# Optimization experiments

Measured on AMD Instinct MI355X. Metric: run time of the kernel, lower is better.

Reference implementation:

```python
import jax, jax.numpy as jnp
import numpy as np
import math

DIM = 128
D_STATE = 16
D_CONV = 4
EXPAND = 2
LFS = 16            # last_feat_size -> H = W = 16, L = 256
IN_IMG = 512
IN_PC = 256
COMB = IN_IMG + IN_PC + 2          # 770
POOL_SCALES = [1, 5, 9, 13]        # arithmetic(1, 16, 4)
NPOOL = len(POOL_SCALES)
D_MODEL = DIM * NPOOL + COMB       # 1282
D_INNER = EXPAND * D_MODEL         # 2564
DT_RANK = math.ceil(D_MODEL / 16)  # 81
B = 64
H = W = LFS


def _ap_mat(insz, outsz):
    # PyTorch AdaptiveAvgPool2d bin weights as a (outsz, insz) matrix
    M = np.zeros((outsz, insz), np.float32)
    for i in range(outsz):
        s = (i * insz) // outsz
        e = -((-(i + 1) * insz) // outsz)  # ceil((i+1)*insz/outsz)
        M[i, s:e] = 1.0 / (e - s)
    return M


def _bl_mat(outsz, insz):
    # bilinear interpolation (align_corners=False) as (outsz, insz) matrix
    M = np.zeros((outsz, insz), np.float32)
    if insz == 1:
        M[:, 0] = 1.0
        return M
    for i in range(outsz):
        src = (i + 0.5) * insz / outsz - 0.5
        src = min(max(src, 0.0), insz - 1.0)
        i0 = int(np.floor(src))
        i1 = min(i0 + 1, insz - 1)
        f = src - i0
        M[i, i0] += 1.0 - f
        M[i, i1] += f
    return M


def setup_inputs():
    key = jax.random.key(0)
    ks = jax.random.split(key, 16)
    def n(k, sh, s=1.0):
        return jax.random.normal(k, sh, jnp.float32) * s
    return {
        'x': n(ks[0], (B, IN_IMG, H, W)),
        'pc_emb': n(ks[1], (B, IN_PC)),
        'conv_w': n(ks[2], (NPOOL, DIM, COMB), 0.05),          # 1x1 convs
        'bn_gamma': jnp.ones((NPOOL, DIM), jnp.float32),
        'bn_beta': jnp.zeros((NPOOL, DIM), jnp.float32),
        'bn_mean': n(ks[3], (NPOOL, DIM), 0.1),
        'bn_var': jax.random.uniform(ks[4], (NPOOL, DIM), jnp.float32, 0.5, 1.5),
        'in_proj_w': n(ks[5], (2 * D_INNER, D_MODEL), D_MODEL ** -0.5),
        'conv1d_w': n(ks[6], (D_INNER, 1, D_CONV), 0.3),       # depthwise causal conv
        'conv1d_b': n(ks[7], (D_INNER,), 0.1),
        'x_proj_w': n(ks[8], (DT_RANK + 2 * D_STATE, D_INNER), D_INNER ** -0.5),
        'dt_proj_w': n(ks[9], (D_INNER, DT_RANK), DT_RANK ** -0.5),
        'dt_proj_b': n(ks[10], (D_INNER,), 0.5) - 3.0,
        'A_log': jnp.log(jax.random.uniform(ks[11], (D_INNER, D_STATE), jnp.float32, 1.0, 16.0)),
        'D': jnp.ones((D_INNER,), jnp.float32),
        'out_proj_w': n(ks[12], (D_MODEL, D_INNER), D_INNER ** -0.5),
    }


def _ppm(x, pc_emb, conv_w, bn_gamma, bn_beta, bn_mean, bn_var):
    Bn = x.shape[0]
    xx = np.linspace(-0.3, 0.3, LFS, dtype=np.float32)
    g = np.stack(np.meshgrid(xx, xx)).reshape(2, LFS, LFS)
    grid = jnp.broadcast_to(jnp.asarray(g)[None], (Bn, 2, H, W))
    pc = jnp.broadcast_to(pc_emb[:, :, None, None], (Bn, IN_PC, H, W))
    comb = jnp.concatenate([x, grid, pc], axis=1)  # (B, COMB, H, W)

    def cbr(i, t):  # 1x1 conv -> BN(eval) -> ReLU6
        y = jnp.einsum('bchw,dc->bdhw', t, conv_w[i])
        inv = jax.lax.rsqrt(bn_var[i] + 1e-5) * bn_gamma[i]
        y = y * inv[None, :, None, None] + (bn_beta[i] - bn_mean[i] * inv)[None, :, None, None]
        return jnp.clip(y, 0.0, 6.0)

    outs = [comb]
    # pool layer 0: ConvBNReLU then AdaptiveAvgPool2d(1); bilinear from 1x1 = broadcast
    y0 = cbr(0, comb).mean(axis=(2, 3), keepdims=True)
    outs.append(jnp.broadcast_to(y0, (Bn, DIM, H, W)))
    for i, s in enumerate(POOL_SCALES[1:], start=1):
        Mp = jnp.asarray(_ap_mat(H, s))
        pooled = jnp.einsum('oh,bchw,pw->bcop', Mp, comb, Mp)  # adaptive avg pool
        y = cbr(i, pooled)
        Mu = jnp.asarray(_bl_mat(H, s))
        outs.append(jnp.einsum('oh,bchw,pw->bcop', Mu, y, Mu))  # bilinear upsample
    return jnp.concatenate(outs, axis=1)  # (B, D_MODEL, H, W)


def _mamba(seq, in_proj_w, conv1d_w, conv1d_b, x_proj_w, dt_proj_w, dt_proj_b, A_log, D, out_proj_w):
    # seq: (B, L, d_model)
    xz = seq @ in_proj_w.T                       # (B, L, 2*d_inner)
    u, z = jnp.split(xz, 2, axis=-1)
    uc = jnp.transpose(u, (0, 2, 1))             # (B, d_inner, L)
    uc = jax.lax.conv_general_dilated(uc, conv1d_w, (1,), [(D_CONV - 1, 0)],
                                      feature_group_count=D_INNER) + conv1d_b[None, :, None]
    u = jax.nn.silu(jnp.transpose(uc, (0, 2, 1)))  # (B, L, d_inner)
    dbl = u @ x_proj_w.T
    dt, Bm, Cm = jnp.split(dbl, [DT_RANK, DT_RANK + D_STATE], axis=-1)
    dt = jax.nn.softplus(dt @ dt_proj_w.T + dt_proj_b)  # (B, L, d_inner)
    A = -jnp.exp(A_log)                                 # (d_inner, d_state)

    def step(h, inp):
        dt_t, B_t, C_t, u_t = inp                # (B,d_inner) (B,N) (B,N) (B,d_inner)
        dA = jnp.exp(dt_t[..., None] * A)        # (B, d_inner, N)
        h = dA * h + (dt_t * u_t)[..., None] * B_t[:, None, :]
        y = jnp.einsum('bdn,bn->bd', h, C_t)
        return h, y

    h0 = jnp.zeros((seq.shape[0], D_INNER, D_STATE), seq.dtype)
    xs = (jnp.moveaxis(dt, 1, 0), jnp.moveaxis(Bm, 1, 0),
          jnp.moveaxis(Cm, 1, 0), jnp.moveaxis(u, 1, 0))
    _, ys = jax.lax.scan(step, h0, xs)
    y = jnp.moveaxis(ys, 0, 1) + u * D
    y = y * jax.nn.silu(z)
    return y @ out_proj_w.T                      # (B, L, d_model)


def reference(x, pc_emb, conv_w, bn_gamma, bn_beta, bn_mean, bn_var,
              in_proj_w, conv1d_w, conv1d_b, x_proj_w, dt_proj_w, dt_proj_b,
              A_log, D, out_proj_w):
    Bn = x.shape[0]
    feat = _ppm(x, pc_emb, conv_w, bn_gamma, bn_beta, bn_mean, bn_var)
    chs = feat.shape[1]
    seq = jnp.transpose(feat.reshape(Bn, chs, H * W), (0, 2, 1))  # b (h w) c
    y = _mamba(seq, in_proj_w, conv1d_w, conv1d_b, x_proj_w,
               dt_proj_w, dt_proj_b, A_log, D, out_proj_w)
    return jnp.transpose(y, (0, 2, 1)).reshape(Bn, chs, H, W)
```

## Files before the change

kernel.cpp:

```cpp
#include <hip/hip_runtime.h>
#include <hip/hip_bf16.h>
#include <math.h>

#define H_ 16
#define W_ 16
#define L_ 256
#define BATCH 64
#define CIMG 512
#define CPC 256
#define COMB_ 770
#define DIMC 128
#define DMODEL 1282
#define DINNER 2564
#define DXZ 5128
#define DTRANK 81
#define NSTATE 16
#define NPOS 275

#define KP_IN 928
#define KBASE 384
#define KP_OUT 2592
#define KP_DT 96
#define NPAD_IN 5248
#define NPAD_OUT 1408
#define NPAD_X 128
#define NPAD_DT 2688
#define XSPLIT 9

typedef __attribute__((ext_vector_type(8))) short short8;
typedef __attribute__((ext_vector_type(4))) float f32x4;

__device__ __forceinline__ float comb_val(const float* __restrict__ x,
                                          const float* __restrict__ pc,
                                          int bg, int c, int h, int w) {
  if (c < CIMG)    return x[(((size_t)bg * CIMG + c) << 8) + (h << 4) + w];
  if (c == CIMG)   return -0.3f + 0.04f * (float)w;
  if (c == CIMG+1) return -0.3f + 0.04f * (float)h;
  return pc[bg * CPC + (c - (CIMG + 2))];
}

__device__ __forceinline__ void split_bf16(float v, unsigned short& h, unsigned short& l) {
  __hip_bfloat16 hb = __float2bfloat16(v);
  h = __builtin_bit_cast(unsigned short, hb);
  float r = v - __bfloat162float(hb);
  __hip_bfloat16 lb = __float2bfloat16(r);
  l = __builtin_bit_cast(unsigned short, lb);
}

__device__ __forceinline__ float bf16_val(unsigned short u) {
  return __bfloat162float(__builtin_bit_cast(__hip_bfloat16, u));
}

__device__ __forceinline__ void idx_to_scale(int idx, int& s, int& o, int& p, int& base) {
  if (idx < 25)       { s = 5;  base = 0; }
  else if (idx < 106) { s = 9;  base = 25; }
  else                { s = 13; base = 106; }
  int r = idx - base;
  o = r / s; p = r - o * s;
}

__global__ __launch_bounds__(256) void wsplit_kernel(
    const float* __restrict__ W, int N, int K,
    unsigned short* __restrict__ Wh, unsigned short* __restrict__ Wl, int Kp) {
  int k = blockIdx.x * 256 + threadIdx.x;
  if (k >= Kp) return;
  int n = blockIdx.y;
  float v = (n < N && k < K) ? W[(size_t)n * K + k] : 0.f;
  unsigned short h, l;
  split_bf16(v, h, l);
  Wh[(size_t)n * Kp + k] = h;
  Wl[(size_t)n * Kp + k] = l;
}

__global__ __launch_bounds__(256) void wsplit_main_kernel(
    const float* __restrict__ W,
    unsigned short* __restrict__ Wh, unsigned short* __restrict__ Wl) {
  int k = blockIdx.x * 256 + threadIdx.x;
  if (k >= KP_IN) return;
  int n = blockIdx.y;
  float v = 0.f;
  if (n < DXZ && k < 898) {
    int src = (k < 514) ? k : k + 384;
    v = W[(size_t)n * DMODEL + src];
  }
  unsigned short h, l;
  split_bf16(v, h, l);
  Wh[(size_t)n * KP_IN + k] = h;
  Wl[(size_t)n * KP_IN + k] = l;
}

__global__ __launch_bounds__(256) void wsplit_base_kernel(
    const float* __restrict__ W,
    unsigned short* __restrict__ Wh, unsigned short* __restrict__ Wl) {
  int k = blockIdx.x * 256 + threadIdx.x;
  if (k >= KBASE) return;
  int n = blockIdx.y;
  float v = (n < DXZ) ? W[(size_t)n * DMODEL + 514 + k] : 0.f;
  unsigned short h, l;
  split_bf16(v, h, l);
  Wh[(size_t)n * KBASE + k] = h;
  Wl[(size_t)n * KBASE + k] = l;
}

__global__ __launch_bounds__(128) void wt_kernel(
    const float* __restrict__ cw, float* __restrict__ Wt) {
  int c = blockIdx.x, i = blockIdx.y, d = threadIdx.x;
  Wt[((size_t)i * COMB_ + c) * DIMC + d] = cw[((size_t)i * DIMC + d) * COMB_ + c];
}

__global__ __launch_bounds__(256) void pool_kernel(
    const float* __restrict__ x, const float* __restrict__ pc,
    float* __restrict__ P, int b0) {
  int t = blockIdx.x * 256 + threadIdx.x;
  if (t >= COMB_ * NPOS) return;
  int bl = blockIdx.y;
  int bg = b0 + bl;
  int c = t / NPOS;
  int idx = t - c * NPOS;
  int s, o, p, base; idx_to_scale(idx, s, o, p, base);
  int hs = (o * 16) / s, he = ((o + 1) * 16 + s - 1) / s;
  int ws2 = (p * 16) / s, we = ((p + 1) * 16 + s - 1) / s;
  float sum = 0.f;
  for (int h = hs; h < he; h++)
    for (int w = ws2; w < we; w++)
      sum += comb_val(x, pc, bg, c, h, w);
  P[((size_t)bl * COMB_ + c) * NPOS + idx] = sum / (float)((he - hs) * (we - ws2));
}

__global__ __launch_bounds__(256) void cbr_pool_a_kernel(
    const float* __restrict__ P, const float* __restrict__ Wt,
    float* __restrict__ Ypar) {
  int tno = blockIdx.x, cg = blockIdx.y, bl = blockIdx.z;
  int i, idx0, cnt;
  if (tno == 0)      { i = 0; idx0 = 0;                cnt = 25; }
  else if (tno < 4)  { i = 1; idx0 = 25 + (tno-1)*32;  cnt = min(32, 106 - idx0); }
  else               { i = 2; idx0 = 106 + (tno-4)*32; cnt = min(32, 275 - idx0); }
  int cbeg = (cg * COMB_) >> 2, cend_ = ((cg + 1) * COMB_) >> 2;
  __shared__ float Ps[64][32];
  __shared__ float Ws[64][128];
  int t = threadIdx.x;
  int dg = t & 31, ig = t >> 5;
  int d0 = dg << 2, ii0 = ig << 2;
  float acc[4][4] = {};
  for (int c0 = cbeg; c0 < cend_; c0 += 64) {
    int cend = min(64, cend_ - c0);
    for (int e = t; e < 64 * 32; e += 256) {
      int cc = e >> 5, ii = e & 31;
      float v = 0.f;
      if (cc < cend && ii < cnt)
        v = P[((size_t)bl * COMB_ + c0 + cc) * NPOS + idx0 + ii];
      Ps[cc][ii] = v;
    }
    for (int e = t; e < 64 * 128; e += 256) {
      int cc = e >> 7, dd = e & 127;
      Ws[cc][dd] = (cc < cend) ? Wt[((size_t)(i + 1) * COMB_ + c0 + cc) * DIMC + dd] : 0.f;
    }
    __syncthreads();
    for (int cc = 0; cc < 64; cc++) {
      f32x4 wv = *(const f32x4*)&Ws[cc][d0];
      f32x4 pv = *(const f32x4*)&Ps[cc][ii0];
      #pragma unroll
      for (int di = 0; di < 4; di++)
        #pragma unroll
        for (int ki = 0; ki < 4; ki++)
          acc[di][ki] += wv[di] * pv[ki];
    }
    __syncthreads();
  }
  size_t cgs = (size_t)cg * BATCH * NPOS * DIMC;
  #pragma unroll
  for (int di = 0; di < 4; di++) {
    #pragma unroll
    for (int ki = 0; ki < 4; ki++) {
      int io = ii0 + ki;
      if (io < cnt)
        Ypar[cgs + ((size_t)bl * NPOS + idx0 + io) * DIMC + d0 + di] = acc[di][ki];
    }
  }
}

__global__ __launch_bounds__(128) void cbr_comb_kernel(
    const float* __restrict__ Ypar,
    const float* __restrict__ gamma, const float* __restrict__ beta,
    const float* __restrict__ mean, const float* __restrict__ var,
    float* __restrict__ Y) {
  int idx = blockIdx.x, bl = blockIdx.y, d = threadIdx.x;
  int i = (idx < 25) ? 1 : (idx < 106 ? 2 : 3);
  size_t cgs = (size_t)BATCH * NPOS * DIMC;
  size_t o = ((size_t)bl * NPOS + idx) * DIMC + d;
  float v = Ypar[o] + Ypar[o + cgs] + Ypar[o + 2 * cgs] + Ypar[o + 3 * cgs];
  int bi = i * DIMC + d;
  float inv = rsqrtf(var[bi] + 1e-5f) * gamma[bi];
  v = v * inv + (beta[bi] - mean[bi] * inv);
  Y[o] = fminf(fmaxf(v, 0.f), 6.f);
}

__global__ __launch_bounds__(256) void cbr0a_kernel(
    const float* __restrict__ x, const float* __restrict__ pc,
    const float* __restrict__ Wt, float* __restrict__ y0c) {
  int tile = blockIdx.x, bl = blockIdx.y;
  int lt = tile & 3, cg = tile >> 2;
  int cbeg = (cg * COMB_) >> 2, cend_ = ((cg + 1) * COMB_) >> 2;
  __shared__ float Cs[64][64];
  __shared__ float Ws[64][128];
  int t = threadIdx.x;
  int dg = t & 31, lg = t >> 5;
  int d0 = dg << 2, l0 = lg << 3;
  float acc[4][8] = {};
  for (int c0 = cbeg; c0 < cend_; c0 += 64) {
    int cn = min(64, cend_ - c0);
    for (int e = t; e < 64 * 64; e += 256) {
      int cc = e >> 6, ll = e & 63;
      float v = 0.f;
      if (cc < cn) {
        int l = lt * 64 + ll;
        v = comb_val(x, pc, bl, c0 + cc, l >> 4, l & 15);
      }
      Cs[cc][ll] = v;
    }
    for (int e = t; e < 64 * 128; e += 256) {
      int cc = e >> 7, dd = e & 127;
      Ws[cc][dd] = (cc < cn) ? Wt[(size_t)(c0 + cc) * DIMC + dd] : 0.f;
    }
    __syncthreads();
    for (int cc = 0; cc < 64; cc++) {
      f32x4 wv = *(const f32x4*)&Ws[cc][d0];
      f32x4 pa = *(const f32x4*)&Cs[cc][l0];
      f32x4 pb = *(const f32x4*)&Cs[cc][l0 + 4];
      #pragma unroll
      for (int di = 0; di < 4; di++) {
        #pragma unroll
        for (int li = 0; li < 4; li++) {
          acc[di][li]     += wv[di] * pa[li];
          acc[di][li + 4] += wv[di] * pb[li];
        }
      }
    }
    __syncthreads();
  }
  #pragma unroll
  for (int di = 0; di < 4; di++)
    #pragma unroll
    for (int li = 0; li < 8; li++)
      y0c[(((size_t)bl * 4 + cg) * 256 + lt * 64 + l0 + li) * DIMC + d0 + di] =
          acc[di][li];
}

__global__ __launch_bounds__(256) void cbr0b_kernel(
    const float* __restrict__ y0c,
    const float* __restrict__ gamma, const float* __restrict__ beta,
    const float* __restrict__ mean, const float* __restrict__ var,
    float* __restrict__ y0s) {
  int bl = blockIdx.x;
  int t = threadIdx.x;
  int d = t & 127, lh = t >> 7;
  float inv = rsqrtf(var[d] + 1e-5f) * gamma[d];
  float bs = beta[d] - mean[d] * inv;
  float s = 0.f;
  size_t cgs = (size_t)256 * DIMC;
  for (int l = lh * 128; l < lh * 128 + 128; l++) {
    size_t base = (((size_t)bl * 4) * 256 + l) * DIMC + d;
    float v = y0c[base] + y0c[base + cgs] + y0c[base + 2 * cgs] + y0c[base + 3 * cgs];
    v = v * inv + bs;
    s += fminf(fmaxf(v, 0.f), 6.f);
  }
  __shared__ float red[256];
  red[t] = s;
  __syncthreads();
  if (t < 128) y0s[bl * DIMC + t] = red[t] + red[t + 128];
}

__global__ __launch_bounds__(256) void pcy0_kernel(
    const float* __restrict__ pc, const float* __restrict__ y0s,
    unsigned short* __restrict__ Abh, unsigned short* __restrict__ Abl) {
  int k = blockIdx.x * 256 + threadIdx.x;
  if (k >= KBASE) return;
  int row = blockIdx.y;
  float v = 0.f;
  if (row < BATCH) {
    if (k < CPC) v = pc[row * CPC + k];
    else v = y0s[(size_t)row * DIMC + (k - CPC)] * (1.f / 256.f);
  }
  unsigned short h, l;
  split_bf16(v, h, l);
  Abh[(size_t)row * KBASE + k] = h;
  Abl[(size_t)row * KBASE + k] = l;
}

__global__ __launch_bounds__(256) void seq_x_kernel(
    const float* __restrict__ x,
    unsigned short* __restrict__ seqh, unsigned short* __restrict__ seql, int b0) {
  int ct = blockIdx.x, ltile = blockIdx.y, bl = blockIdx.z;
  int bg = b0 + bl;
  __shared__ float Ct[64][65];
  int t = threadIdx.x;
  int c0 = ct << 6, l0 = ltile << 6;
  for (int e = t; e < 64 * 64; e += 256) {
    int cc = e >> 6, ll = e & 63;
    Ct[ll][cc] = x[(((size_t)bg * CIMG + c0 + cc) << 8) + l0 + ll];
  }
  __syncthreads();
  int r = t >> 2, cq = (t & 3) << 4;
  size_t rb = ((size_t)bl * L_ + l0 + r) * KP_IN + c0 + cq;
  short8 h0, h1, lo0, lo1;
  #pragma unroll
  for (int k = 0; k < 8; k++) {
    unsigned short hh, ll;
    split_bf16(Ct[r][cq + k], hh, ll);
    h0[k] = (short)hh; lo0[k] = (short)ll;
  }
  #pragma unroll
  for (int k = 0; k < 8; k++) {
    unsigned short hh, ll;
    split_bf16(Ct[r][cq + 8 + k], hh, ll);
    h1[k] = (short)hh; lo1[k] = (short)ll;
  }
  *(short8*)&seqh[rb]     = h0;
  *(short8*)&seqh[rb + 8] = h1;
  *(short8*)&seql[rb]     = lo0;
  *(short8*)&seql[rb + 8] = lo1;
}

__global__ __launch_bounds__(256) void seq_rest_kernel(
    const float* __restrict__ x, const float* __restrict__ pc,
    const float* __restrict__ Y,
    unsigned short* __restrict__ seqh, unsigned short* __restrict__ seql, int b0) {
  int l = blockIdx.x, bl = blockIdx.y, bg = b0 + bl;
  int h = l >> 4, w = l & 15;
  size_t rb = ((size_t)bl * L_ + l) * KP_IN;
  for (int c = 512 + threadIdx.x; c < KP_IN; c += 256) {
    float v;
    if (c < CIMG + 2) {
      v = comb_val(x, pc, bg, c, h, w);
    } else if (c < 898) {
      int cc = c - 514;
      int si = cc >> 7;
      int d = cc & 127;
      int s    = (si == 0) ? 5 : ((si == 1) ? 9 : 13);
      int base = (si == 0) ? 0 : ((si == 1) ? 25 : 106);
      float srch = (h + 0.5f) * (float)s * (1.f / 16.f) - 0.5f;
      srch = fminf(fmaxf(srch, 0.f), (float)(s - 1));
      int o0 = (int)floorf(srch);
      float fh = srch - (float)o0;
      int o1 = min(o0 + 1, s - 1);
      float srcw = (w + 0.5f) * (float)s * (1.f / 16.f) - 0.5f;
      srcw = fminf(fmaxf(srcw, 0.f), (float)(s - 1));
      int p0 = (int)floorf(srcw);
      float fw = srcw - (float)p0;
      int p1 = min(p0 + 1, s - 1);
      const float* Yb = &Y[((size_t)bg * NPOS + base) * DIMC + d];
      float v00 = Yb[(size_t)(o0 * s + p0) * DIMC];
      float v01 = Yb[(size_t)(o0 * s + p1) * DIMC];
      float v10 = Yb[(size_t)(o1 * s + p0) * DIMC];
      float v11 = Yb[(size_t)(o1 * s + p1) * DIMC];
      v = (1.f - fh) * ((1.f - fw) * v00 + fw * v01)
        +        fh  * ((1.f - fw) * v10 + fw * v11);
    } else {
      v = 0.f;
    }
    unsigned short hh, ll;
    split_bf16(v, hh, ll);
    seqh[rb + c] = hh;
    seql[rb + c] = ll;
  }
}

__global__ __launch_bounds__(256) void mfma_gemm_kernel(
    const unsigned short* __restrict__ Ah, const unsigned short* __restrict__ Al, int Kp,
    const unsigned short* __restrict__ Bh, const unsigned short* __restrict__ Bl,
    float* __restrict__ C, int ldc, int M, int N, int mode,
    const float* __restrict__ bias,
    float* __restrict__ outT, int b0, size_t czstr) {
  __shared__ __align__(16) unsigned short Sbuf[2][4][128 * 32];
  int tid = threadIdx.x;
  int lane = tid & 63;
  int wave = tid >> 6;

  int kn = Kp / (int)gridDim.z;
  int kbeg = (int)blockIdx.z * kn;
  int nt = kn >> 5;
  C += (size_t)blockIdx.z * czstr;

  int gx = gridDim.x, gy = gridDim.y;
  int lin = blockIdx.y * gx + blockIdx.x;
  int total = gx * gy;
  int mt, nt_;
  if ((total & 7) == 0) {
    int vid = (lin & 7) * (total >> 3) + (lin >> 3);
    mt = vid % gy; nt_ = vid / gy;
  } else {
    mt = blockIdx.y; nt_ = blockIdx.x;
  }
  int m0 = mt << 7, n0 = nt_ << 7;
  int wm = (wave & 1) << 6, wn = (wave >> 1) << 6;
  f32x4 acc[4][4] = {};
  int mrow = lane & 15;
  int kx = (((lane >> 4) ^ ((lane >> 2) & 3)) << 3);

  auto STAGE = [&](int ph, int k0) {
    #pragma unroll
    for (int j = 0; j < 2; j++) {
      int c = (j << 8) + tid;
      int r = c >> 2;
      int kc = (((c & 3) ^ ((r >> 2) & 3)) << 3);
      size_t ga = (size_t)(m0 + r) * Kp + k0 + kc;
      size_t gb = (size_t)(n0 + r) * Kp + k0 + kc;
      __builtin_amdgcn_global_load_lds(
          (const __attribute__((address_space(1))) unsigned int*)(Ah + ga),
          (__attribute__((address_space(3))) unsigned int*)(&Sbuf[ph][0][c << 3]), 16, 0, 0);
      __builtin_amdgcn_global_load_lds(
          (const __attribute__((address_space(1))) unsigned int*)(Al + ga),
          (__attribute__((address_space(3))) unsigned int*)(&Sbuf[ph][1][c << 3]), 16, 0, 0);
      __builtin_amdgcn_global_load_lds(
          (const __attribute__((address_space(1))) unsigned int*)(Bh + gb),
          (__attribute__((address_space(3))) unsigned int*)(&Sbuf[ph][2][c << 3]), 16, 0, 0);
      __builtin_amdgcn_global_load_lds(
          (const __attribute__((address_space(1))) unsigned int*)(Bl + gb),
          (__attribute__((address_space(3))) unsigned int*)(&Sbuf[ph][3][c << 3]), 16, 0, 0);
    }
  };

  STAGE(0, kbeg);
  __syncthreads();
  int cur = 0;
  for (int t = 0; t < nt; t++) {
    if (t + 1 < nt) STAGE(cur ^ 1, kbeg + ((t + 1) << 5));
    short8 ah[4], al[4], bh[4], blo[4];
    #pragma unroll
    for (int i = 0; i < 4; i++) {
      int ro = (wm + (i << 4) + mrow) * 32 + kx;
      ah[i] = *(const short8*)&Sbuf[cur][0][ro];
      al[i] = *(const short8*)&Sbuf[cur][1][ro];
    }
    #pragma unroll
    for (int j = 0; j < 4; j++) {
      int ro = (wn + (j << 4) + mrow) * 32 + kx;
      bh[j]  = *(const short8*)&Sbuf[cur][2][ro];
      blo[j] = *(const short8*)&Sbuf[cur][3][ro];
    }
    #pragma unroll
    for (int i = 0; i < 4; i++)
      #pragma unroll
      for (int j = 0; j < 4; j++) {
        acc[i][j] = __builtin_amdgcn_mfma_f32_16x16x32_bf16(ah[i], bh[j],  acc[i][j], 0, 0, 0);
        acc[i][j] = __builtin_amdgcn_mfma_f32_16x16x32_bf16(ah[i], blo[j], acc[i][j], 0, 0, 0);
        acc[i][j] = __builtin_amdgcn_mfma_f32_16x16x32_bf16(al[i], bh[j],  acc[i][j], 0, 0, 0);
      }
    __syncthreads();
    cur ^= 1;
  }

  int n_l = lane & 15, m_l = (lane >> 4) << 2;
  #pragma unroll
  for (int i = 0; i < 4; i++) {
    int gm0 = m0 + wm + (i << 4) + m_l;
    #pragma unroll
    for (int j = 0; j < 4; j++) {
      int gn = n0 + wn + (j << 4) + n_l;
      if (gn >= N) continue;
      if (mode == 2) {
        int bb = b0 + (gm0 >> 8), l0 = gm0 & 255;
        *(f32x4*)&outT[(((size_t)bb * DMODEL + gn) << 8) + l0] = acc[i][j];
      } else if (mode == 1) {
        float bv = bias[gn];
        #pragma unroll
        for (int r = 0; r < 4; r++) {
          float vv = acc[i][j][r] + bv;
          vv = (vv > 20.f) ? vv : log1pf(expf(vv));
          C[(size_t)(gm0 + r) * ldc + gn] = vv;
        }
      } else if (mode == 3) {
        float bv = bias[(size_t)(b0 + (gm0 >> 8)) * DXZ + gn];
        if (gn < DINNER) {
          #pragma unroll
          for (int r = 0; r < 4; r++)
            C[(size_t)(gm0 + r) * DINNER + gn] = acc[i][j][r] + bv;
        } else {
          int g2 = gn - DINNER;
          #pragma unroll
          for (int r = 0; r < 4; r++)
            outT[(size_t)(gm0 + r) * DINNER + g2] = acc[i][j][r] + bv;
        }
      } else {
        #pragma unroll
        for (int r = 0; r < 4; r++)
          C[(size_t)(gm0 + r) * ldc + gn] = acc[i][j][r];
      }
    }
  }
}

__global__ __launch_bounds__(256) void conv1d_kernel(
    const float* __restrict__ U, const float* __restrict__ cw,
    const float* __restrict__ cb,
    unsigned short* __restrict__ vh, unsigned short* __restrict__ vl) {
  int d = blockIdx.x * 256 + threadIdx.x;
  if (d >= KP_OUT) return;
  int m0 = blockIdx.y << 2;
  if (d >= DINNER) {
    #pragma unroll
    for (int q = 0; q < 4; q++) {
      size_t o = (size_t)(m0 + q) * KP_OUT + d;
      vh[o] = 0; vl[o] = 0;
    }
    return;
  }
  int bbase = m0 & ~255;
  float xr[7];
  #pragma unroll
  for (int k = 0; k < 7; k++) {
    int r = m0 - 3 + k;
    xr[k] = (r >= bbase) ? U[(size_t)r * DINNER + d] : 0.f;
  }
  float w0 = cw[d * 4], w1 = cw[d * 4 + 1], w2 = cw[d * 4 + 2], w3 = cw[d * 4 + 3];
  float b = cb[d];
  #pragma unroll
  for (int q = 0; q < 4; q++) {
    float acc = b + w0 * xr[q] + w1 * xr[q + 1] + w2 * xr[q + 2] + w3 * xr[q + 3];
    float s = acc / (1.f + __expf(-acc));
    unsigned short hh, llv;
    split_bf16(s, hh, llv);
    size_t o = (size_t)(m0 + q) * KP_OUT + d;
    vh[o] = hh; vl[o] = llv;
  }
}

__global__ __launch_bounds__(256) void split_bc_kernel(
    const float* __restrict__ dbl, size_t zstr,
    unsigned short* __restrict__ dth, unsigned short* __restrict__ dtl,
    float* __restrict__ bcs, int Mtot) {
  int t = blockIdx.x * 256 + threadIdx.x;
  int m = t >> 7, k = t & 127;
  if (m >= Mtot) return;
  const float* p = dbl + (size_t)m * 128;
  if (k < KP_DT) {
    float v = 0.f;
    if (k < DTRANK) {
      #pragma unroll
      for (int q = 0; q < XSPLIT; q++) v += p[(size_t)q * zstr + k];
    }
    unsigned short h, l;
    split_bf16(v, h, l);
    dth[(size_t)m * KP_DT + k] = h;
    dtl[(size_t)m * KP_DT + k] = l;
  } else {
    int n = k - KP_DT;
    float v = 0.f;
    #pragma unroll
    for (int q = 0; q < XSPLIT; q++) v += p[(size_t)q * zstr + DTRANK + n];
    bcs[(size_t)m * 32 + n] = v;
  }
}

__global__ __launch_bounds__(256) void scan_kernel(
    const float* __restrict__ dtv,
    const unsigned short* __restrict__ vh, const unsigned short* __restrict__ vl,
    const float* __restrict__ Z,
    const float* __restrict__ bcs, const float* __restrict__ A_log,
    const float* __restrict__ Dv,
    unsigned short* __restrict__ yh, unsigned short* __restrict__ yl) {
  int dl = threadIdx.x & 63;
  int s  = threadIdx.x >> 6;
  int d  = (blockIdx.x << 6) + dl;
  int bl = blockIdx.y;
  bool valid = d < DINNER;
  bool wout  = d < KP_OUT;
  int de = valid ? d : (DINNER - 1);
  __shared__ float Sh[3][64][NSTATE];
  __shared__ float Sp[3][64][NSTATE];
  float A[NSTATE], h[NSTATE];
  #pragma unroll
  for (int n = 0; n < NSTATE; n++) {
    A[n] = -__expf(A_log[de * NSTATE + n]);
    h[n] = 0.f;
  }
  float Dd = Dv[de];
  size_t mb = (size_t)bl * L_ + (s << 6);
  if (s < 3) {
    float sdt = 0.f;
    for (int i = 0; i < 64; i++) {
      size_t m = mb + i;
      float dt = dtv[m * DINNER + de];
      float uu = bf16_val(vh[m * KP_OUT + de]) + bf16_val(vl[m * KP_OUT + de]);
      const f32x4* bp = (const f32x4*)&bcs[m * 32];
      f32x4 b4a = bp[0], b4b = bp[1], b4c = bp[2], b4d = bp[3];
      float du = dt * uu;
      sdt += dt;
      #pragma unroll
      for (int n = 0; n < NSTATE; n++) {
        float bv = (n < 4) ? b4a[n & 3] : (n < 8) ? b4b[n & 3]
                 : (n < 12) ? b4c[n & 3] : b4d[n & 3];
        h[n] = __expf(dt * A[n]) * h[n] + du * bv;
      }
    }
    #pragma unroll
    for (int n = 0; n < NSTATE; n++) {
      Sh[s][dl][n] = h[n];
      Sp[s][dl][n] = __expf(A[n] * sdt);
    }
  }
  __syncthreads();
  #pragma unroll
  for (int n = 0; n < NSTATE; n++) h[n] = 0.f;
  for (int t = 0; t < s; t++)
    #pragma unroll
    for (int n = 0; n < NSTATE; n++)
      h[n] = Sp[t][dl][n] * h[n] + Sh[t][dl][n];
  for (int i = 0; i < 64; i++) {
    size_t m = mb + i;
    float dt = dtv[m * DINNER + de];
    float uu = bf16_val(vh[m * KP_OUT + de]) + bf16_val(vl[m * KP_OUT + de]);
    float zz = Z[m * DINNER + de];
    const f32x4* bp = (const f32x4*)&bcs[m * 32];
    f32x4 b4a = bp[0], b4b = bp[1], b4c = bp[2], b4d = bp[3];
    f32x4 c4a = bp[4], c4b = bp[5], c4c = bp[6], c4d = bp[7];
    float du = dt * uu;
    float y = 0.f;
    #pragma unroll
    for (int n = 0; n < NSTATE; n++) {
      float bv = (n < 4) ? b4a[n & 3] : (n < 8) ? b4b[n & 3]
               : (n < 12) ? b4c[n & 3] : b4d[n & 3];
      float cv = (n < 4) ? c4a[n & 3] : (n < 8) ? c4b[n & 3]
               : (n < 12) ? c4c[n & 3] : c4d[n & 3];
      h[n] = __expf(dt * A[n]) * h[n] + du * bv;
      y += h[n] * cv;
    }
    float val = (y + uu * Dd) * (zz / (1.f + __expf(-zz)));
    if (!valid) val = 0.f;
    if (wout) {
      unsigned short hh, ll;
      split_bf16(val, hh, ll);
      yh[m * KP_OUT + d] = hh;
      yl[m * KP_OUT + d] = ll;
    }
  }
}

extern "C" void kernel_launch(void* const* d_in, const int* in_sizes, int n_in,
                              void* d_out, int out_size, void* d_ws, size_t ws_size,
                              hipStream_t stream) {
  const float* x         = (const float*)d_in[0];
  const float* pc        = (const float*)d_in[1];
  const float* conv_w    = (const float*)d_in[2];
  const float* bn_gamma  = (const float*)d_in[3];
  const float* bn_beta   = (const float*)d_in[4];
  const float* bn_mean   = (const float*)d_in[5];
  const float* bn_var    = (const float*)d_in[6];
  const float* in_proj_w = (const float*)d_in[7];
  const float* conv1d_w  = (const float*)d_in[8];
  const float* conv1d_b  = (const float*)d_in[9];
  const float* x_proj_w  = (const float*)d_in[10];
  const float* dt_proj_w = (const float*)d_in[11];
  const float* dt_proj_b = (const float*)d_in[12];
  const float* A_log     = (const float*)d_in[13];
  const float* Dvec      = (const float*)d_in[14];
  const float* out_proj_w= (const float*)d_in[15];
  float* out = (float*)d_out;

  auto al = [](size_t vv) { return (vv + 255) & ~(size_t)255; };

  size_t w_in_sz  = al((size_t)NPAD_IN * KP_IN * 2);
  size_t w_b_sz   = al((size_t)NPAD_IN * KBASE * 2);
  size_t w_out_sz = al((size_t)NPAD_OUT * KP_OUT * 2);
  size_t w_x_sz   = al((size_t)NPAD_X * KP_OUT * 2);
  size_t w_d_sz   = al((size_t)NPAD_DT * KP_DT * 2);
  size_t wt_sz    = al((size_t)4 * COMB_ * DIMC * 4);
  size_t y0s_sz   = al((size_t)BATCH * DIMC * 4);
  size_t ab_sz    = al((size_t)128 * KBASE * 2);
  size_t cb_sz    = al((size_t)128 * DXZ * 4);
  size_t yf_sz    = al((size_t)BATCH * NPOS * DIMC * 4);
  size_t p_sz     = al((size_t)BATCH * COMB_ * NPOS * 4);
  size_t y0c_sz   = al((size_t)BATCH * 4 * 256 * DIMC * 4);
  size_t ypar_sz  = al((size_t)4 * BATCH * NPOS * DIMC * 4);

  char* base = (char*)d_ws;
  size_t off = 0;
  auto take = [&](size_t sz) { void* r = base + off; off += sz; return r; };
  unsigned short* Wih = (unsigned short*)take(w_in_sz);
  unsigned short* Wil = (unsigned short*)take(w_in_sz);
  unsigned short* Wbh = (unsigned short*)take(w_b_sz);
  unsigned short* Wbl = (unsigned short*)take(w_b_sz);
  unsigned short* Woh = (unsigned short*)take(w_out_sz);
  unsigned short* Wol = (unsigned short*)take(w_out_sz);
  unsigned short* Wxh = (unsigned short*)take(w_x_sz);
  unsigned short* Wxl = (unsigned short*)take(w_x_sz);
  unsigned short* Wdh = (unsigned short*)take(w_d_sz);
  unsigned short* Wdl = (unsigned short*)take(w_d_sz);
  float* Wt    = (float*)take(wt_sz);
  float* y0s   = (float*)take(y0s_sz);
  unsigned short* Abh = (unsigned short*)take(ab_sz);
  unsigned short* Abl = (unsigned short*)take(ab_sz);
  float* Cbase = (float*)take(cb_sz);
  float* Yf    = (float*)take(yf_sz);
  char* arena  = base + off;

  size_t pro_need = p_sz + y0c_sz + ypar_sz;
  auto chunk = [&](int bc) -> size_t {
    size_t Mcb = (size_t)bc * L_;
    size_t hyb = al(Mcb * KP_OUT * 2);
    size_t s = 2 * hyb
             + 2 * al(Mcb * DINNER * 4)
             + 2 * al(Mcb * KP_OUT * 2)
             + al((size_t)XSPLIT * Mcb * 128 * 4)
             + al(Mcb * 32 * 4)
             + 2 * al(Mcb * KP_DT * 2);
    return s < pro_need ? pro_need : s;
  };
  int Bc = 64;
  while (Bc > 1 && off + chunk(Bc) > ws_size) Bc >>= 1;

  size_t Mc = (size_t)Bc * L_;
  size_t hy = al(Mc * KP_OUT * 2);
  size_t zstr = Mc * 128;
  size_t aoff = 0;
  auto takeA = [&](size_t sz) { void* r = arena + aoff; aoff += sz; return r; };
  float* P    = (float*)arena;
  float* y0c  = (float*)(arena + p_sz);
  float* Ypar = (float*)(arena + p_sz + y0c_sz);
  unsigned short* seqh = (unsigned short*)takeA(hy);
  unsigned short* seql = (unsigned short*)takeA(hy);
  float* U   = (float*)takeA(al(Mc * DINNER * 4));
  float* Z   = (float*)takeA(al(Mc * DINNER * 4));
  unsigned short* vhb = (unsigned short*)takeA(al(Mc * KP_OUT * 2));
  unsigned short* vlb = (unsigned short*)takeA(al(Mc * KP_OUT * 2));
  float* dblb = (float*)takeA(al((size_t)XSPLIT * Mc * 128 * 4));
  float* bcs  = (float*)takeA(al(Mc * 32 * 4));
  unsigned short* dth = (unsigned short*)takeA(al(Mc * KP_DT * 2));
  unsigned short* dtl = (unsigned short*)takeA(al(Mc * KP_DT * 2));
  unsigned short* yhb = seqh;
  unsigned short* ylb = seql;
  float* dtb = U;

  wsplit_main_kernel<<<dim3((KP_IN + 255) / 256, NPAD_IN), 256, 0, stream>>>(
      in_proj_w, Wih, Wil);
  wsplit_base_kernel<<<dim3((KBASE + 255) / 256, NPAD_IN), 256, 0, stream>>>(
      in_proj_w, Wbh, Wbl);
  wsplit_kernel<<<dim3((KP_OUT + 255) / 256, NPAD_OUT), 256, 0, stream>>>(
      out_proj_w, DMODEL, DINNER, Woh, Wol, KP_OUT);
  wsplit_kernel<<<dim3((KP_OUT + 255) / 256, NPAD_X), 256, 0, stream>>>(
      x_proj_w, DTRANK + 2 * NSTATE, DINNER, Wxh, Wxl, KP_OUT);
  wsplit_kernel<<<dim3((KP_DT + 255) / 256, NPAD_DT), 256, 0, stream>>>(
      dt_proj_w, DINNER, DTRANK, Wdh, Wdl, KP_DT);
  wt_kernel<<<dim3(COMB_, 4), 128, 0, stream>>>(conv_w, Wt);

  pool_kernel<<<dim3((COMB_ * NPOS + 255) / 256, BATCH), 256, 0, stream>>>(x, pc, P, 0);
  cbr_pool_a_kernel<<<dim3(10, 4, BATCH), 256, 0, stream>>>(P, Wt, Ypar);
  cbr_comb_kernel<<<dim3(NPOS, BATCH), 128, 0, stream>>>(Ypar, bn_gamma, bn_beta,
                                                         bn_mean, bn_var, Yf);
  cbr0a_kernel<<<dim3(16, BATCH), 256, 0, stream>>>(x, pc, Wt, y0c);
  cbr0b_kernel<<<dim3(BATCH), 256, 0, stream>>>(y0c, bn_gamma, bn_beta,
                                                bn_mean, bn_var, y0s);
  pcy0_kernel<<<dim3((KBASE + 255) / 256, 128), 256, 0, stream>>>(pc, y0s, Abh, Abl);
  mfma_gemm_kernel<<<dim3(NPAD_IN / 128, 1, 1), 256, 0, stream>>>(
      Abh, Abl, KBASE, Wbh, Wbl, Cbase, DXZ, 128, DXZ, 0, nullptr, nullptr, 0, 0);

  for (int b0 = 0; b0 < BATCH; b0 += Bc) {
    int Mci = (int)Mc;
    seq_x_kernel<<<dim3(8, 4, Bc), 256, 0, stream>>>(x, seqh, seql, b0);
    seq_rest_kernel<<<dim3(L_, Bc), 256, 0, stream>>>(x, pc, Yf, seqh, seql, b0);
    mfma_gemm_kernel<<<dim3(NPAD_IN / 128, Mci / 128, 1), 256, 0, stream>>>(
        seqh, seql, KP_IN, Wih, Wil, U, DINNER, Mci, DXZ, 3, Cbase, Z, b0, 0);
    conv1d_kernel<<<dim3((KP_OUT + 255) / 256, Mci / 4), 256, 0, stream>>>(
        U, conv1d_w, conv1d_b, vhb, vlb);
    mfma_gemm_kernel<<<dim3(1, Mci / 128, XSPLIT), 256, 0, stream>>>(
        vhb, vlb, KP_OUT, Wxh, Wxl, dblb, 128, Mci, DTRANK + 2 * NSTATE, 0,
        nullptr, nullptr, 0, zstr);
    split_bc_kernel<<<dim3(Mci / 2), 256, 0, stream>>>(dblb, zstr, dth, dtl, bcs, Mci);
    mfma_gemm_kernel<<<dim3(NPAD_DT / 128, Mci / 128, 1), 256, 0, stream>>>(
        dth, dtl, KP_DT, Wdh, Wdl, dtb, DINNER, Mci, DINNER, 1, dt_proj_b,
        nullptr, 0, 0);
    scan_kernel<<<dim3(41, Bc), 256, 0, stream>>>(
        dtb, vhb, vlb, Z, bcs, A_log, Dvec, yhb, ylb);
    mfma_gemm_kernel<<<dim3(NPAD_OUT / 128, Mci / 128, 1), 256, 0, stream>>>(
        yhb, ylb, KP_OUT, Woh, Wol, nullptr, 0, Mci, DMODEL, 2, nullptr, out, b0, 0);
  }
}
```

Before: 2.615 ms.

## Load A-low operand directly from global and retile block swizzle into bands

The split-bf16 GEMM stops staging the low half of A through LDS; each lane loads its Al fragment straight from global memory into registers, which shrinks the LDS buffer from four to three slabs. The Al-based MFMAs are moved into a separate loop after the other products, giving the global loads time to land. The block-to-tile mapping gains a banded swizzle, grouping 8 M-tiles per band, to improve L2 reuse. The cost is uncoalesced per-lane global loads in the inner loop and added latency exposure if those loads are not hidden.

```diff
diff --git a/kernel.cpp b/kernel.cpp
--- a/kernel.cpp
+++ b/kernel.cpp
@@ -371,21 +371,28 @@
     float* __restrict__ C, int ldc, int M, int N, int mode,
     const float* __restrict__ bias,
     float* __restrict__ outT, int b0, size_t czstr) {
-  __shared__ __align__(16) unsigned short Sbuf[2][4][128 * 32];
+  __shared__ __align__(16) unsigned short Sbuf[2][3][128 * 32];
   int tid = threadIdx.x;
   int lane = tid & 63;
   int wave = tid >> 6;
 
   int kn = Kp / (int)gridDim.z;
   int kbeg = (int)blockIdx.z * kn;
-  int nt = kn >> 5;
+  int nsteps = kn >> 5;
   C += (size_t)blockIdx.z * czstr;
 
   int gx = gridDim.x, gy = gridDim.y;
   int lin = blockIdx.y * gx + blockIdx.x;
   int total = gx * gy;
   int mt, nt_;
-  if ((total & 7) == 0) {
+  if ((total & 7) == 0 && (gy & 7) == 0) {
+    int vid = (lin & 7) * (total >> 3) + (lin >> 3);
+    int S = gx << 3;
+    int band = vid / S;
+    int r = vid - band * S;
+    nt_ = r >> 3;
+    mt = (band << 3) + (r & 7);
+  } else if ((total & 7) == 0) {
     int vid = (lin & 7) * (total >> 3) + (lin >> 3);
     mt = vid % gy; nt_ = vid / gy;
   } else {
@@ -396,6 +403,7 @@
   f32x4 acc[4][4] = {};
   int mrow = lane & 15;
   int kx = (((lane >> 4) ^ ((lane >> 2) & 3)) << 3);
+  int kg = (lane >> 4) << 3;
 
   auto STAGE = [&](int ph, int k0) {
     #pragma unroll
@@ -409,34 +417,35 @@
           (const __attribute__((address_space(1))) unsigned int*)(Ah + ga),
           (__attribute__((address_space(3))) unsigned int*)(&Sbuf[ph][0][c << 3]), 16, 0, 0);
       __builtin_amdgcn_global_load_lds(
-          (const __attribute__((address_space(1))) unsigned int*)(Al + ga),
+          (const __attribute__((address_space(1))) unsigned int*)(Bh + gb),
           (__attribute__((address_space(3))) unsigned int*)(&Sbuf[ph][1][c << 3]), 16, 0, 0);
       __builtin_amdgcn_global_load_lds(
-          (const __attribute__((address_space(1))) unsigned int*)(Bh + gb),
+          (const __attribute__((address_space(1))) unsigned int*)(Bl + gb),
           (__attribute__((address_space(3))) unsigned int*)(&Sbuf[ph][2][c << 3]), 16, 0, 0);
-      __builtin_amdgcn_global_load_lds(
-          (const __attribute__((address_space(1))) unsigned int*)(Bl + gb),
-          (__attribute__((address_space(3))) unsigned int*)(&Sbuf[ph][3][c << 3]), 16, 0, 0);
     }
   };
 
   STAGE(0, kbeg);
   __syncthreads();
   int cur = 0;
-  for (int t = 0; t < nt; t++) {
-    if (t + 1 < nt) STAGE(cur ^ 1, kbeg + ((t + 1) << 5));
-    short8 ah[4], al[4], bh[4], blo[4];
+  for (int t = 0; t < nsteps; t++) {
+    int k0 = kbeg + (t << 5);
+    if (t + 1 < nsteps) STAGE(cur ^ 1, k0 + 32);
+    short8 alr[4];
+    #pragma unroll
+    for (int i = 0; i < 4; i++)
+      alr[i] = *(const short8*)&Al[(size_t)(m0 + wm + (i << 4) + mrow) * Kp + k0 + kg];
+    short8 ah[4], bh[4], blo[4];
     #pragma unroll
     for (int i = 0; i < 4; i++) {
       int ro = (wm + (i << 4) + mrow) * 32 + kx;
       ah[i] = *(const short8*)&Sbuf[cur][0][ro];
-      al[i] = *(const short8*)&Sbuf[cur][1][ro];
     }
     #pragma unroll
     for (int j = 0; j < 4; j++) {
       int ro = (wn + (j << 4) + mrow) * 32 + kx;
-      bh[j]  = *(const short8*)&Sbuf[cur][2][ro];
-      blo[j] = *(const short8*)&Sbuf[cur][3][ro];
+      bh[j]  = *(const short8*)&Sbuf[cur][1][ro];
+      blo[j] = *(const short8*)&Sbuf[cur][2][ro];
     }
     #pragma unroll
     for (int i = 0; i < 4; i++)
@@ -444,8 +453,12 @@
       for (int j = 0; j < 4; j++) {
         acc[i][j] = __builtin_amdgcn_mfma_f32_16x16x32_bf16(ah[i], bh[j],  acc[i][j], 0, 0, 0);
         acc[i][j] = __builtin_amdgcn_mfma_f32_16x16x32_bf16(ah[i], blo[j], acc[i][j], 0, 0, 0);
-        acc[i][j] = __builtin_amdgcn_mfma_f32_16x16x32_bf16(al[i], bh[j],  acc[i][j], 0, 0, 0);
       }
+    #pragma unroll
+    for (int i = 0; i < 4; i++)
+      #pragma unroll
+      for (int j = 0; j < 4; j++)
+        acc[i][j] = __builtin_amdgcn_mfma_f32_16x16x32_bf16(alr[i], bh[j], acc[i][j], 0, 0, 0);
     __syncthreads();
     cur ^= 1;
   }
```

Measured after the change: 2.623 ms. No clear change (+0.3%).
